# Kernel optimization log

Measured on AMD Instinct MI355X. Metric: run time of the kernel, lower is better.

The kernel has to match this reference:

```python
import jax, jax.numpy as jnp
import numpy as np

C = 512
M = 8            # n_heads
G = 32           # GroupNorm groups
EPS = 1e-6


def setup_inputs() -> dict:
    key = jax.random.key(0)
    ks = jax.random.split(key, 7)
    x = jax.random.normal(ks[0], (2, C, 64, 64), dtype=jnp.float32)
    gn_weight = jnp.ones((C,), jnp.float32)
    gn_bias = jnp.zeros((C,), jnp.float32)
    qkv_w = jax.random.normal(ks[1], (3 * C, C), jnp.float32) * (1.0 / np.sqrt(C))
    qkv_b = jnp.zeros((3 * C,), jnp.float32)
    # source zero-inits proj_out; we use small random weights so the attention
    proj_w = jax.random.normal(ks[2], (C, C), jnp.float32) * (0.02 / np.sqrt(C))
    proj_b = jnp.zeros((C,), jnp.float32)
    return {"x": x, "gn_weight": gn_weight, "gn_bias": gn_bias,
            "qkv_w": qkv_w, "qkv_b": qkv_b, "proj_w": proj_w, "proj_b": proj_b}


def _forward(x, gn_weight, gn_bias, qkv_w, qkv_b, proj_w, proj_b):
    b, c, H, W = x.shape
    n = H * W
    d = c // M
    xf = x.reshape(b, c, n)

    # GroupNorm(32, c, eps=1e-6, affine)
    xg = xf.reshape(b, G, (c // G) * n)
    mu = xg.mean(axis=-1, keepdims=True)
    var = xg.var(axis=-1, keepdims=True)
    xn = ((xg - mu) * jax.lax.rsqrt(var + EPS)).reshape(b, c, n)
    xn = xn * gn_weight[None, :, None] + gn_bias[None, :, None]

    # 1x1 conv -> qkv, then legacy reshape-then-split
    qkv = jnp.einsum('oc,bcn->bon', qkv_w, xn) + qkv_b[None, :, None]  # (b, 3c, n)
    qkv = qkv.reshape(b * M, 3 * d, n)
    q, k, v = qkv[:, :d], qkv[:, d:2 * d], qkv[:, 2 * d:]

    scale = 1.0 / np.sqrt(np.sqrt(d))
    w = jnp.einsum('Bdi,Bdj->Bij', q * scale, k * scale)  # (b*m, n, n)
    w = jax.nn.softmax(w, axis=-1)
    a = jnp.einsum('Bin,Bdn->Bdi', w, v)                  # (b*m, d, n)
    a = a.reshape(b, c, n)

    h = jnp.einsum('oc,bcn->bon', proj_w, a) + proj_b[None, :, None]
    # NOTE: source reassigns x = norm(x) before the residual add.
    return (xn + h).reshape(b, c, H, W)


def reference(x, gn_weight, gn_bias, qkv_w, qkv_b, proj_w, proj_b):
    return _forward(x, gn_weight, gn_bias, qkv_w, qkv_b, proj_w, proj_b)
```

## Files before the change

kernel.cpp:

```cpp
#include <hip/hip_runtime.h>
#include <cstdint>
#include <cstddef>

typedef __attribute__((ext_vector_type(8))) short short8;
typedef __attribute__((ext_vector_type(4))) float f32x4;

#define QSCALE 0.18033688011112043f

__device__ __forceinline__ float bf2f(unsigned short u) {
  return __uint_as_float(((unsigned)u) << 16);
}
__device__ __forceinline__ unsigned short f2bf(float f) {
  unsigned u = __float_as_uint(f);
  u += 0x7fffu + ((u >> 16) & 1u);
  return (unsigned short)(u >> 16);
}
__device__ __forceinline__ unsigned cvtpk(float a, float b) {
  unsigned r;
  asm("v_cvt_pk_bf16_f32 %0, %1, %2" : "=v"(r) : "v"(a), "v"(b));
  return r;
}
__device__ __forceinline__ short8 mk8(unsigned a, unsigned b, unsigned c, unsigned d) {
  union { unsigned u[4]; short8 s; } x;
  x.u[0] = a; x.u[1] = b; x.u[2] = c; x.u[3] = d;
  return x.s;
}
__device__ __forceinline__ void g2l16(const void* g, void* l) {
  __builtin_amdgcn_global_load_lds(
      (const __attribute__((address_space(1))) unsigned int*)g,
      (__attribute__((address_space(3))) unsigned int*)l, 16, 0, 0);
}

__global__ __launch_bounds__(256) void k_wgn(const float* __restrict__ wqf,
                                             const float* __restrict__ wpf,
                                             unsigned short* __restrict__ wq,
                                             unsigned short* __restrict__ wp,
                                             const float* __restrict__ x,
                                             float* __restrict__ part) {
  __shared__ float red[8];
  const int blk = blockIdx.x;
  const int t = threadIdx.x;
  if (blk < 1024) {
    int i = blk * 256 + t;
    if (i < 196608) {
      float4 v = ((const float4*)wqf)[i];
      ushort4 u;
      u.x = f2bf(v.x); u.y = f2bf(v.y); u.z = f2bf(v.z); u.w = f2bf(v.w);
      ((ushort4*)wq)[i] = u;
    } else {
      int k = i - 196608;
      float4 v = ((const float4*)wpf)[k];
      ushort4 u;
      u.x = f2bf(v.x); u.y = f2bf(v.y); u.z = f2bf(v.z); u.w = f2bf(v.w);
      ((ushort4*)wp)[k] = u;
    }
  } else {
    int b2 = blk - 1024;
    int bg = b2 >> 4, slice = b2 & 15;
    const float4* base = (const float4*)(x + (size_t)bg * 65536 + (size_t)slice * 4096);
    float s = 0.f, q = 0.f;
#pragma unroll
    for (int i = 0; i < 4; ++i) {
      float4 v = base[t + i * 256];
      s += v.x + v.y + v.z + v.w;
      q += v.x * v.x + v.y * v.y + v.z * v.z + v.w * v.w;
    }
#pragma unroll
    for (int off = 1; off < 64; off <<= 1) {
      s += __shfl_xor(s, off);
      q += __shfl_xor(q, off);
    }
    int wid = t >> 6;
    if ((t & 63) == 0) { red[wid * 2] = s; red[wid * 2 + 1] = q; }
    __syncthreads();
    if (t == 0) {
      float S = red[0] + red[2] + red[4] + red[6];
      float Q = red[1] + red[3] + red[5] + red[7];
      part[b2 * 2] = S;
      part[b2 * 2 + 1] = Q;
    }
  }
}

__global__ void k_gnfin(const float* __restrict__ part, float* __restrict__ stats) {
  int t = threadIdx.x;
  float S = 0.f, Q = 0.f;
#pragma unroll
  for (int i = 0; i < 16; ++i) {
    S += part[(t * 16 + i) * 2];
    Q += part[(t * 16 + i) * 2 + 1];
  }
  float mean = S * (1.f / 65536.f);
  float var = Q * (1.f / 65536.f) - mean * mean;
  stats[t * 2] = mean;
  stats[t * 2 + 1] = rsqrtf(var + 1e-6f);
}

__global__ __launch_bounds__(256) void k_gnnorm(const float* __restrict__ x,
                                                const float* __restrict__ gnw,
                                                const float* __restrict__ gnb,
                                                const float* __restrict__ stats,
                                                unsigned short* __restrict__ xn,
                                                unsigned short* __restrict__ xnT) {
  __shared__ float T[64 * 65];
  const int t = threadIdx.x;
  const int n0 = blockIdx.x * 64, c0 = blockIdx.y * 64, bb = blockIdx.z;
#pragma unroll
  for (int p = 0; p < 4; ++p) {
    int s = p * 256 + t;
    int row = s >> 4, seg = s & 15;
    int c = c0 + row;
    int gi = bb * 32 + (c >> 4);
    float mean = stats[gi * 2], rstd = stats[gi * 2 + 1];
    float gw = gnw[c] * rstd;
    float gb = gnb[c] - mean * gw;
    float4 v = *(const float4*)(x + ((size_t)bb * 512 + c) * 4096 + n0 + seg * 4);
    float f0 = v.x * gw + gb, f1 = v.y * gw + gb, f2 = v.z * gw + gb, f3 = v.w * gw + gb;
    ushort4 u;
    u.x = f2bf(f0); u.y = f2bf(f1); u.z = f2bf(f2); u.w = f2bf(f3);
    *(ushort4*)(xn + ((size_t)bb * 512 + c) * 4096 + n0 + seg * 4) = u;
    T[(seg * 4 + 0) * 65 + row] = f0;
    T[(seg * 4 + 1) * 65 + row] = f1;
    T[(seg * 4 + 2) * 65 + row] = f2;
    T[(seg * 4 + 3) * 65 + row] = f3;
  }
  __syncthreads();
#pragma unroll
  for (int p = 0; p < 4; ++p) {
    int s = p * 256 + t;
    int nl = s >> 4, cs = s & 15;
    float f0 = T[nl * 65 + cs * 4 + 0];
    float f1 = T[nl * 65 + cs * 4 + 1];
    float f2 = T[nl * 65 + cs * 4 + 2];
    float f3 = T[nl * 65 + cs * 4 + 3];
    ushort4 u;
    u.x = f2bf(f0); u.y = f2bf(f1); u.z = f2bf(f2); u.w = f2bf(f3);
    *(ushort4*)(xnT + ((size_t)bb * 4096 + n0 + nl) * 512 + c0 + cs * 4) = u;
  }
}

template <int MODE>
__global__ __launch_bounds__(256) void k_gemm(
    const unsigned short* __restrict__ A,
    const unsigned short* __restrict__ Bt,
    const float* __restrict__ bias,
    unsigned short* __restrict__ outA,
    unsigned short* __restrict__ outT,
    const unsigned short* __restrict__ resid,
    float* __restrict__ outF,
    int Mo) {
  __shared__ char lds[34816];
  const int t = threadIdx.x;
  const int lane = t & 63;
  const int g = lane >> 4, ln = lane & 15;
  const int wid = t >> 6, wr = wid >> 1, wc = wid & 1;
  const int bn0 = blockIdx.x * 128, bm0 = blockIdx.y * 128, bb = blockIdx.z;

  const unsigned short* Ab = A + (size_t)bm0 * 512;
  const unsigned short* Bb = Bt + ((size_t)bb * 4096 + bn0) * 512;

  f32x4 acc[4][4];
#pragma unroll
  for (int m = 0; m < 4; ++m)
#pragma unroll
    for (int n = 0; n < 4; ++n) acc[m][n] = f32x4{0.f, 0.f, 0.f, 0.f};

#pragma unroll 1
  for (int kt = 0; kt < 8; ++kt) {
#pragma unroll
    for (int p = 0; p < 4; ++p) {
      int s = p * 256 + t;
      int row = s >> 3;
      int csg = (s & 7) ^ (row & 7);
      g2l16(Ab + (size_t)row * 512 + kt * 64 + csg * 8,
            &lds[(p * 256 + (t & ~63)) * 16]);
    }
#pragma unroll
    for (int p = 0; p < 4; ++p) {
      int s = p * 256 + t;
      int row = s >> 3;
      int csg = (s & 7) ^ (row & 7);
      g2l16(Bb + (size_t)row * 512 + kt * 64 + csg * 8,
            &lds[16384 + (p * 256 + (t & ~63)) * 16]);
    }
    __syncthreads();
#pragma unroll
    for (int kk = 0; kk < 2; ++kk) {
      short8 af[4], bfr[4];
#pragma unroll
      for (int m = 0; m < 4; ++m) {
        int row = wr * 64 + m * 16 + ln;
        int cs = (kk * 4 + g) ^ (row & 7);
        af[m] = *(const short8*)&lds[row * 128 + cs * 16];
      }
#pragma unroll
      for (int n = 0; n < 4; ++n) {
        int row = wc * 64 + n * 16 + ln;
        int cs = (kk * 4 + g) ^ (row & 7);
        bfr[n] = *(const short8*)&lds[16384 + row * 128 + cs * 16];
      }
      __builtin_amdgcn_s_setprio(1);
#pragma unroll
      for (int m = 0; m < 4; ++m)
#pragma unroll
        for (int n = 0; n < 4; ++n)
          acc[m][n] = __builtin_amdgcn_mfma_f32_16x16x32_bf16(af[m], bfr[n], acc[m][n], 0, 0, 0);
      __builtin_amdgcn_s_setprio(0);
    }
    __syncthreads();
  }

  if (MODE == 0) {
#pragma unroll
    for (int m = 0; m < 4; ++m)
#pragma unroll
      for (int n = 0; n < 4; ++n)
#pragma unroll
        for (int r = 0; r < 4; ++r) {
          int ol = wr * 64 + m * 16 + g * 4 + r;
          int jl = wc * 64 + n * 16 + ln;
          int o = bm0 + ol, j = bn0 + jl;
          float v = acc[m][n][r] + bias[o];
          unsigned short bv = f2bf(v);
          if ((o % 192) >= 128) {
            int jp = (j & ~63) | (j & 32) | ((j & 0xC) << 1) | ((j & 16) >> 2) | (j & 3);
            outA[((size_t)bb * 1536 + o) * 4096 + jp] = bv;
          }
          *(unsigned short*)&lds[jl * 272 + ol * 2] = bv;
        }
    __syncthreads();
#pragma unroll
    for (int p = 0; p < 8; ++p) {
      int s = p * 256 + t;
      int jl = s >> 4, cs = s & 15;
      int oo = bm0 + cs * 8;
      if ((oo % 192) < 128) {
        short8 v = *(const short8*)&lds[jl * 272 + cs * 16];
        *(short8*)&outT[((size_t)bb * 4096 + bn0 + jl) * 1536 + oo] = v;
      }
    }
  } else {
#pragma unroll
    for (int m = 0; m < 4; ++m)
#pragma unroll
      for (int n = 0; n < 4; ++n)
#pragma unroll
        for (int r = 0; r < 4; ++r) {
          int o = bm0 + wr * 64 + m * 16 + g * 4 + r;
          int j = bn0 + wc * 64 + n * 16 + ln;
          size_t idx = ((size_t)bb * 512 + o) * 4096 + j;
          outF[idx] = acc[m][n][r] + bias[o] + bf2f(resid[idx]);
        }
  }
}

__global__ __launch_bounds__(256, 2) void k_attn(const unsigned short* __restrict__ qkv,
                                                 const unsigned short* __restrict__ qkvT,
                                                 unsigned short* __restrict__ aT) {
  __shared__ char lds[49152];
  const int t = threadIdx.x, lane = t & 63;
  const int g = lane >> 4, ln = lane & 15;
  const int wid = t >> 6;
  const int qw = wid >> 1;
  const int jw = wid & 1;
  const int h = blockIdx.y, bb = blockIdx.z;
  const int q0 = blockIdx.x * 128 + qw * 64;

  int kaddr[2][2], vaddr[4];
#pragma unroll
  for (int kk = 0; kk < 2; ++kk)
#pragma unroll
    for (int jf = 0; jf < 2; ++jf) {
      int row = jw * 32 + jf * 16 + ln;
      kaddr[kk][jf] = row * 128 + (((kk * 4 + g) ^ (row & 7)) << 4);
    }
#pragma unroll
  for (int df = 0; df < 4; ++df) {
    int row = df * 16 + ln;
    vaddr[df] = 24576 + row * 128 + (((jw * 4 + g) ^ (row & 7)) << 4);
  }

  const unsigned short* kS[2];
  const unsigned short* vS[2];
  int ldst[2];
#pragma unroll
  for (int p = 0; p < 2; ++p) {
    int s = p * 256 + t;
    int row = s >> 3, csg = (s & 7) ^ (row & 7);
    kS[p] = qkvT + ((size_t)bb * 4096 + row) * 1536 + 192 * h + 64 + csg * 8;
    vS[p] = qkv + ((size_t)bb * 1536 + 192 * h + 128 + row) * 4096 + csg * 8;
    ldst[p] = (p * 256 + (t & ~63)) * 16;
  }

  short8 qf[4][2];
#pragma unroll
  for (int qt = 0; qt < 4; ++qt)
#pragma unroll
    for (int kk = 0; kk < 2; ++kk) {
      short8 v = *(const short8*)(qkvT + ((size_t)bb * 4096 + q0 + qt * 16 + ln) * 1536 +
                                  192 * h + kk * 32 + g * 8);
#pragma unroll
      for (int e = 0; e < 8; ++e) {
        float f = bf2f((unsigned short)v[e]) * QSCALE;
        v[e] = (short)f2bf(f);
      }
      qf[qt][kk] = v;
    }

  const short8 onesb = mk8(0x3F803F80u, 0x3F803F80u, 0x3F803F80u, 0x3F803F80u);

  f32x4 acc[4][4];
  f32x4 lacc[4];
#pragma unroll
  for (int qt = 0; qt < 4; ++qt) {
#pragma unroll
    for (int df = 0; df < 4; ++df) acc[qt][df] = f32x4{0.f, 0.f, 0.f, 0.f};
    lacc[qt] = f32x4{0.f, 0.f, 0.f, 0.f};
  }

#pragma unroll
  for (int jt = 0; jt < 2; ++jt) {
#pragma unroll
    for (int p = 0; p < 2; ++p) {
      g2l16(kS[p], &lds[jt * 8192 + ldst[p]]);
      g2l16(vS[p], &lds[24576 + jt * 8192 + ldst[p]]);
      kS[p] += 64 * 1536;
      vS[p] += 64;
    }
  }

#pragma unroll 3
  for (int jt = 0; jt < 64; ++jt) {
    const int cur = jt % 3;
    const char* Kc = &lds[cur * 8192];
    if (jt < 63) {
      asm volatile("s_waitcnt vmcnt(4) lgkmcnt(0)" ::: "memory");
    } else {
      asm volatile("s_waitcnt vmcnt(0) lgkmcnt(0)" ::: "memory");
    }
    __builtin_amdgcn_s_barrier();
    __builtin_amdgcn_sched_barrier(0);

    if (jt < 62) {
      int nb = (jt + 2) % 3;
#pragma unroll
      for (int p = 0; p < 2; ++p) {
        g2l16(kS[p], &lds[nb * 8192 + ldst[p]]);
        g2l16(vS[p], &lds[24576 + nb * 8192 + ldst[p]]);
        kS[p] += 64 * 1536;
        vS[p] += 64;
      }
    }

    short8 kf[2][2];
#pragma unroll
    for (int kk = 0; kk < 2; ++kk)
#pragma unroll
      for (int jf = 0; jf < 2; ++jf) kf[kk][jf] = *(const short8*)(Kc + kaddr[kk][jf]);

    const f32x4 zf = f32x4{0.f, 0.f, 0.f, 0.f};
    f32x4 w[4][2];
    __builtin_amdgcn_s_setprio(1);
#pragma unroll
    for (int qt = 0; qt < 4; ++qt)
#pragma unroll
      for (int jf = 0; jf < 2; ++jf)
        w[qt][jf] = __builtin_amdgcn_mfma_f32_16x16x32_bf16(kf[0][jf], qf[qt][0], zf, 0, 0, 0);
#pragma unroll
    for (int qt = 0; qt < 4; ++qt)
#pragma unroll
      for (int jf = 0; jf < 2; ++jf)
        w[qt][jf] = __builtin_amdgcn_mfma_f32_16x16x32_bf16(kf[1][jf], qf[qt][1], w[qt][jf], 0, 0, 0);
    __builtin_amdgcn_s_setprio(0);

    short8 vf[4];
#pragma unroll
    for (int df = 0; df < 4; ++df) vf[df] = *(const short8*)(Kc + vaddr[df]);

#pragma unroll
    for (int qt = 0; qt < 4; ++qt)
#pragma unroll
      for (int jf = 0; jf < 2; ++jf)
#pragma unroll
        for (int r = 0; r < 4; ++r) w[qt][jf][r] = __builtin_amdgcn_exp2f(w[qt][jf][r]);

    short8 pf[4];
#pragma unroll
    for (int qt = 0; qt < 4; ++qt)
      pf[qt] = mk8(cvtpk(w[qt][0][0], w[qt][0][1]),
                   cvtpk(w[qt][0][2], w[qt][0][3]),
                   cvtpk(w[qt][1][0], w[qt][1][1]),
                   cvtpk(w[qt][1][2], w[qt][1][3]));

    __builtin_amdgcn_s_setprio(1);
#pragma unroll
    for (int qt = 0; qt < 4; ++qt) {
#pragma unroll
      for (int df = 0; df < 4; ++df)
        acc[qt][df] = __builtin_amdgcn_mfma_f32_16x16x32_bf16(pf[qt], vf[df], acc[qt][df], 0, 0, 0);
      lacc[qt] = __builtin_amdgcn_mfma_f32_16x16x32_bf16(pf[qt], onesb, lacc[qt], 0, 0, 0);
    }
    __builtin_amdgcn_s_setprio(0);
  }

  __syncthreads();
  float* cb = (float*)lds;
  const int cbase = qw * 5120;
  if (jw == 1) {
#pragma unroll
    for (int qt = 0; qt < 4; ++qt) {
#pragma unroll
      for (int df = 0; df < 4; ++df)
        *(f32x4*)&cb[cbase + ((qt * 4 + df) * 64 + lane) * 4] = acc[qt][df];
      *(f32x4*)&cb[cbase + 4096 + (qt * 64 + lane) * 4] = lacc[qt];
    }
  }
  __syncthreads();
  if (jw == 0) {
#pragma unroll
    for (int qt = 0; qt < 4; ++qt) {
#pragma unroll
      for (int df = 0; df < 4; ++df)
        acc[qt][df] += *(const f32x4*)&cb[cbase + ((qt * 4 + df) * 64 + lane) * 4];
      lacc[qt] += *(const f32x4*)&cb[cbase + 4096 + (qt * 64 + lane) * 4];
    }
#pragma unroll
    for (int qt = 0; qt < 4; ++qt)
#pragma unroll
      for (int r = 0; r < 4; ++r) {
        float inv = 1.f / lacc[qt][r];
        int row = q0 + qt * 16 + g * 4 + r;
#pragma unroll
        for (int df = 0; df < 4; ++df)
          aT[((size_t)bb * 4096 + row) * 512 + h * 64 + df * 16 + ln] =
              f2bf(acc[qt][df][r] * inv);
      }
  }
}

extern "C" void kernel_launch(void* const* d_in, const int* in_sizes, int n_in,
                              void* d_out, int out_size, void* d_ws, size_t ws_size,
                              hipStream_t stream) {
  const float* x     = (const float*)d_in[0];
  const float* gnw   = (const float*)d_in[1];
  const float* gnb   = (const float*)d_in[2];
  const float* qkvw  = (const float*)d_in[3];
  const float* qkvb  = (const float*)d_in[4];
  const float* projw = (const float*)d_in[5];
  const float* projb = (const float*)d_in[6];
  float* out = (float*)d_out;
  char* ws = (char*)d_ws;

  const size_t OFF_WQ   = 0;
  const size_t OFF_WP   = 1572864;
  const size_t OFF_XN   = 2097152;
  const size_t OFF_XNT  = 10485760;
  const size_t OFF_QKV  = 18874368;
  const size_t OFF_QKVT = 44040192;
  const size_t OFF_AT   = 69206016;
  const size_t OFF_PART = 77594624;
  const size_t OFF_STAT = 77602816;

  unsigned short* wq   = (unsigned short*)(ws + OFF_WQ);
  unsigned short* wp   = (unsigned short*)(ws + OFF_WP);
  unsigned short* xn   = (unsigned short*)(ws + OFF_XN);
  unsigned short* xnT  = (unsigned short*)(ws + OFF_XNT);
  unsigned short* qkv  = (unsigned short*)(ws + OFF_QKV);
  unsigned short* qkvT = (unsigned short*)(ws + OFF_QKVT);
  unsigned short* aT   = (unsigned short*)(ws + OFF_AT);
  float* part  = (float*)(ws + OFF_PART);
  float* stats = (float*)(ws + OFF_STAT);

  k_wgn<<<dim3(2048), dim3(256), 0, stream>>>(qkvw, projw, wq, wp, x, part);
  k_gnfin<<<dim3(1), dim3(64), 0, stream>>>(part, stats);
  k_gnnorm<<<dim3(64, 8, 2), dim3(256), 0, stream>>>(x, gnw, gnb, stats, xn, xnT);
  k_gemm<0><<<dim3(32, 12, 2), dim3(256), 0, stream>>>(wq, xnT, qkvb, qkv, qkvT, nullptr, nullptr, 1536);
  k_attn<<<dim3(32, 8, 2), dim3(256), 0, stream>>>(qkv, qkvT, aT);
  k_gemm<1><<<dim3(32, 4, 2), dim3(256), 0, stream>>>(wp, aT, projb, nullptr, nullptr, xn, out, 512);
}
```

Measured before the change: 125.0 us.

## Use 128-key tiles with double buffering in attention kernel

The attention main loop now processes 128 keys per iteration instead of 64, moving from a triple-buffered 64-key ring to a double-buffered 128-key pipeline in 64KB of LDS. The V tile layout is widened to 256-byte rows with a 16-way XOR swizzle, and the S=QK^T / exp / PV work is split into two halves to limit register pressure. The goal is to halve the number of barriers and loop iterations and amortize the LDS loads over more MFMAs. In exchange, the wait is now a full vmcnt(0), so the prefetch has less slack. The larger LDS footprint and register use may also lower occupancy below the two blocks per CU requested.

```diff
diff --git a/kernel.cpp b/kernel.cpp
--- a/kernel.cpp
+++ b/kernel.cpp
@@ -257,7 +257,7 @@
 __global__ __launch_bounds__(256, 2) void k_attn(const unsigned short* __restrict__ qkv,
                                                  const unsigned short* __restrict__ qkvT,
                                                  unsigned short* __restrict__ aT) {
-  __shared__ char lds[49152];
+  __shared__ char lds[65536];
   const int t = threadIdx.x, lane = t & 63;
   const int g = lane >> 4, ln = lane & 15;
   const int wid = t >> 6;
@@ -266,30 +266,36 @@
   const int h = blockIdx.y, bb = blockIdx.z;
   const int q0 = blockIdx.x * 128 + qw * 64;
 
-  int kaddr[2][2], vaddr[4];
+  int kaddr[2][4];
 #pragma unroll
   for (int kk = 0; kk < 2; ++kk)
 #pragma unroll
-    for (int jf = 0; jf < 2; ++jf) {
-      int row = jw * 32 + jf * 16 + ln;
+    for (int jf = 0; jf < 4; ++jf) {
+      int row = jw * 64 + jf * 16 + ln;
       kaddr[kk][jf] = row * 128 + (((kk * 4 + g) ^ (row & 7)) << 4);
     }
-#pragma unroll
-  for (int df = 0; df < 4; ++df) {
-    int row = df * 16 + ln;
-    vaddr[df] = 24576 + row * 128 + (((jw * 4 + g) ^ (row & 7)) << 4);
-  }
-
-  const unsigned short* kS[2];
-  const unsigned short* vS[2];
-  int ldst[2];
-#pragma unroll
-  for (int p = 0; p < 2; ++p) {
+  int vaddr[2][4];
+#pragma unroll
+  for (int kk2 = 0; kk2 < 2; ++kk2)
+#pragma unroll
+    for (int df = 0; df < 4; ++df) {
+      int row = df * 16 + ln;
+      int c = (jw * 8 + kk2 * 4 + g) ^ (row & 15);
+      vaddr[kk2][df] = 16384 + row * 256 + c * 16;
+    }
+
+  const unsigned short* kS[4];
+  const unsigned short* vS[4];
+  int ldstK[4], ldstV[4];
+#pragma unroll
+  for (int p = 0; p < 4; ++p) {
     int s = p * 256 + t;
-    int row = s >> 3, csg = (s & 7) ^ (row & 7);
-    kS[p] = qkvT + ((size_t)bb * 4096 + row) * 1536 + 192 * h + 64 + csg * 8;
-    vS[p] = qkv + ((size_t)bb * 1536 + 192 * h + 128 + row) * 4096 + csg * 8;
-    ldst[p] = (p * 256 + (t & ~63)) * 16;
+    int rowK = s >> 3, csgK = (s & 7) ^ (rowK & 7);
+    kS[p] = qkvT + ((size_t)bb * 4096 + rowK) * 1536 + 192 * h + 64 + csgK * 8;
+    ldstK[p] = (p * 256 + (t & ~63)) * 16;
+    int rowV = s >> 4, csgV = (s & 15) ^ (rowV & 15);
+    vS[p] = qkv + ((size_t)bb * 1536 + 192 * h + 128 + rowV) * 4096 + csgV * 8;
+    ldstV[p] = 16384 + (p * 256 + (t & ~63)) * 16;
   }
 
   short8 qf[4][2];
@@ -319,86 +325,91 @@
   }
 
 #pragma unroll
-  for (int jt = 0; jt < 2; ++jt) {
-#pragma unroll
-    for (int p = 0; p < 2; ++p) {
-      g2l16(kS[p], &lds[jt * 8192 + ldst[p]]);
-      g2l16(vS[p], &lds[24576 + jt * 8192 + ldst[p]]);
-      kS[p] += 64 * 1536;
-      vS[p] += 64;
-    }
-  }
-
-#pragma unroll 3
-  for (int jt = 0; jt < 64; ++jt) {
-    const int cur = jt % 3;
-    const char* Kc = &lds[cur * 8192];
-    if (jt < 63) {
-      asm volatile("s_waitcnt vmcnt(4) lgkmcnt(0)" ::: "memory");
-    } else {
-      asm volatile("s_waitcnt vmcnt(0) lgkmcnt(0)" ::: "memory");
-    }
+  for (int p = 0; p < 4; ++p) {
+    g2l16(kS[p], &lds[ldstK[p]]);
+    g2l16(vS[p], &lds[ldstV[p]]);
+    kS[p] += 128 * 1536;
+    vS[p] += 128;
+  }
+
+#pragma unroll 2
+  for (int jt = 0; jt < 32; ++jt) {
+    const int cur = jt & 1;
+    const char* B = &lds[cur * 32768];
+    asm volatile("s_waitcnt vmcnt(0) lgkmcnt(0)" ::: "memory");
     __builtin_amdgcn_s_barrier();
     __builtin_amdgcn_sched_barrier(0);
 
-    if (jt < 62) {
-      int nb = (jt + 2) % 3;
-#pragma unroll
-      for (int p = 0; p < 2; ++p) {
-        g2l16(kS[p], &lds[nb * 8192 + ldst[p]]);
-        g2l16(vS[p], &lds[24576 + nb * 8192 + ldst[p]]);
-        kS[p] += 64 * 1536;
-        vS[p] += 64;
-      }
-    }
-
-    short8 kf[2][2];
+    if (jt < 31) {
+      int nb = cur ^ 1;
+#pragma unroll
+      for (int p = 0; p < 4; ++p) {
+        g2l16(kS[p], &lds[nb * 32768 + ldstK[p]]);
+        g2l16(vS[p], &lds[nb * 32768 + ldstV[p]]);
+        kS[p] += 128 * 1536;
+        vS[p] += 128;
+      }
+    }
+
+    short8 kf[2][4];
 #pragma unroll
     for (int kk = 0; kk < 2; ++kk)
 #pragma unroll
-      for (int jf = 0; jf < 2; ++jf) kf[kk][jf] = *(const short8*)(Kc + kaddr[kk][jf]);
+      for (int jf = 0; jf < 4; ++jf) kf[kk][jf] = *(const short8*)(B + kaddr[kk][jf]);
+
+    short8 vf[2][4];
+#pragma unroll
+    for (int kk2 = 0; kk2 < 2; ++kk2)
+#pragma unroll
+      for (int df = 0; df < 4; ++df) vf[kk2][df] = *(const short8*)(B + vaddr[kk2][df]);
 
     const f32x4 zf = f32x4{0.f, 0.f, 0.f, 0.f};
-    f32x4 w[4][2];
+    short8 pf[4][2];
+#pragma unroll
+    for (int half = 0; half < 2; ++half) {
+      f32x4 w[2][4];
+      __builtin_amdgcn_s_setprio(1);
+#pragma unroll
+      for (int q2 = 0; q2 < 2; ++q2)
+#pragma unroll
+        for (int jf = 0; jf < 4; ++jf)
+          w[q2][jf] = __builtin_amdgcn_mfma_f32_16x16x32_bf16(kf[0][jf], qf[half * 2 + q2][0],
+                                                              zf, 0, 0, 0);
+#pragma unroll
+      for (int q2 = 0; q2 < 2; ++q2)
+#pragma unroll
+        for (int jf = 0; jf < 4; ++jf)
+          w[q2][jf] = __builtin_amdgcn_mfma_f32_16x16x32_bf16(kf[1][jf], qf[half * 2 + q2][1],
+                                                              w[q2][jf], 0, 0, 0);
+      __builtin_amdgcn_s_setprio(0);
+#pragma unroll
+      for (int q2 = 0; q2 < 2; ++q2)
+#pragma unroll
+        for (int jf = 0; jf < 4; ++jf)
+#pragma unroll
+          for (int r = 0; r < 4; ++r) w[q2][jf][r] = __builtin_amdgcn_exp2f(w[q2][jf][r]);
+#pragma unroll
+      for (int q2 = 0; q2 < 2; ++q2)
+#pragma unroll
+        for (int kk2 = 0; kk2 < 2; ++kk2)
+          pf[half * 2 + q2][kk2] =
+              mk8(cvtpk(w[q2][2 * kk2][0], w[q2][2 * kk2][1]),
+                  cvtpk(w[q2][2 * kk2][2], w[q2][2 * kk2][3]),
+                  cvtpk(w[q2][2 * kk2 + 1][0], w[q2][2 * kk2 + 1][1]),
+                  cvtpk(w[q2][2 * kk2 + 1][2], w[q2][2 * kk2 + 1][3]));
+    }
+
     __builtin_amdgcn_s_setprio(1);
 #pragma unroll
-    for (int qt = 0; qt < 4; ++qt)
-#pragma unroll
-      for (int jf = 0; jf < 2; ++jf)
-        w[qt][jf] = __builtin_amdgcn_mfma_f32_16x16x32_bf16(kf[0][jf], qf[qt][0], zf, 0, 0, 0);
-#pragma unroll
-    for (int qt = 0; qt < 4; ++qt)
-#pragma unroll
-      for (int jf = 0; jf < 2; ++jf)
-        w[qt][jf] = __builtin_amdgcn_mfma_f32_16x16x32_bf16(kf[1][jf], qf[qt][1], w[qt][jf], 0, 0, 0);
-    __builtin_amdgcn_s_setprio(0);
-
-    short8 vf[4];
-#pragma unroll
-    for (int df = 0; df < 4; ++df) vf[df] = *(const short8*)(Kc + vaddr[df]);
-
-#pragma unroll
-    for (int qt = 0; qt < 4; ++qt)
-#pragma unroll
-      for (int jf = 0; jf < 2; ++jf)
-#pragma unroll
-        for (int r = 0; r < 4; ++r) w[qt][jf][r] = __builtin_amdgcn_exp2f(w[qt][jf][r]);
-
-    short8 pf[4];
-#pragma unroll
-    for (int qt = 0; qt < 4; ++qt)
-      pf[qt] = mk8(cvtpk(w[qt][0][0], w[qt][0][1]),
-                   cvtpk(w[qt][0][2], w[qt][0][3]),
-                   cvtpk(w[qt][1][0], w[qt][1][1]),
-                   cvtpk(w[qt][1][2], w[qt][1][3]));
-
-    __builtin_amdgcn_s_setprio(1);
-#pragma unroll
     for (int qt = 0; qt < 4; ++qt) {
 #pragma unroll
-      for (int df = 0; df < 4; ++df)
-        acc[qt][df] = __builtin_amdgcn_mfma_f32_16x16x32_bf16(pf[qt], vf[df], acc[qt][df], 0, 0, 0);
-      lacc[qt] = __builtin_amdgcn_mfma_f32_16x16x32_bf16(pf[qt], onesb, lacc[qt], 0, 0, 0);
+      for (int kk2 = 0; kk2 < 2; ++kk2) {
+#pragma unroll
+        for (int df = 0; df < 4; ++df)
+          acc[qt][df] = __builtin_amdgcn_mfma_f32_16x16x32_bf16(pf[qt][kk2], vf[kk2][df],
+                                                                acc[qt][df], 0, 0, 0);
+        lacc[qt] = __builtin_amdgcn_mfma_f32_16x16x32_bf16(pf[qt][kk2], onesb, lacc[qt], 0, 0, 0);
+      }
     }
     __builtin_amdgcn_s_setprio(0);
   }
```

Result: no change. 126.4 us (+1.1%).
